# Kernel optimization log

Hardware: AMD Instinct MI355X
Metric: run time of the kernel (lower is better)

Reference implementation:

```python
import jax, jax.numpy as jnp
import numpy as np

B, C, N, L, LAYERS = 32, 128, 307, 12, 4
LH = L + 1  # high-frequency channel time length after left-pad
BN_EPS = 1e-5


def _temporal_attention(seq, c1w, c2w, w, b, v, gamma, beta):
    # seq: [B, C, N, T]
    # conv1 (1x1 over channel dim) -> f1: [B, T, N]
    f1 = jnp.einsum('bcnt,c->btn', seq, c1w)
    # conv2 (1x1 over node dim)    -> f2: [B, T, C]
    f2 = jnp.einsum('bcnt,n->btc', seq, c2w)
    # scores = sigmoid(f1 @ w @ f2^T + b): [B, T, T]
    f1w = jnp.einsum('btn,nc->btc', f1, w)
    scores = jax.nn.sigmoid(jnp.einsum('btc,bqc->btq', f1w, f2) + b)
    # learned mixing: v @ scores
    logits = jnp.einsum('tk,bkq->btq', v, scores)
    # BatchNorm1d over tem_size channels (channel = last axis q after the
    # permute(0,2,1) in the torch code); training-mode batch statistics
    mean = logits.mean(axis=(0, 1), keepdims=True)
    var = ((logits - mean) ** 2).mean(axis=(0, 1), keepdims=True)
    logits = (logits - mean) * jax.lax.rsqrt(var + BN_EPS) * gamma + beta
    coefs = jax.nn.softmax(logits, axis=-1)  # [B, T, Q]
    # x_1 = einsum('bcnl,blq->bcnq', seq, coefs^T)
    return jnp.einsum('bcnt,bqt->bcnq', seq, coefs)


def _make_params(key, c, n, t, layers):
    ks = jax.random.split(key, 4)
    return dict(
        c1=jax.random.normal(ks[0], (layers, c), jnp.float32) * 0.05,
        c2=jax.random.normal(ks[1], (layers, n), jnp.float32) * 0.05,
        w=jax.random.normal(ks[2], (layers, n, c), jnp.float32) * 0.05,
        b=jnp.zeros((layers, t, t), jnp.float32),
        v=jax.random.normal(ks[3], (layers, t, t), jnp.float32) * 0.2,
        g=jnp.ones((layers, t), jnp.float32),
        beta=jnp.zeros((layers, t), jnp.float32),
    )


def setup_inputs():
    key = jax.random.key(0)
    k0, k1, k2, k3 = jax.random.split(key, 4)
    XL = jax.random.normal(k0, (B, C, N, L), jnp.float32)
    XH = jax.random.normal(k1, (B, C, N, L), jnp.float32)
    low = _make_params(k2, C, N, L, LAYERS)
    high = _make_params(k3, C, N, LH, LAYERS)
    return {
        'XL': XL, 'XH': XH,
        'low_c1': low['c1'], 'low_c2': low['c2'], 'low_w': low['w'],
        'low_b': low['b'], 'low_v': low['v'], 'low_g': low['g'], 'low_beta': low['beta'],
        'high_c1': high['c1'], 'high_c2': high['c2'], 'high_w': high['w'],
        'high_b': high['b'], 'high_v': high['v'], 'high_g': high['g'], 'high_beta': high['beta'],
        'alpha': jnp.array(-5.0, jnp.float32),
    }


def reference(XL, XH, low_c1, low_c2, low_w, low_b, low_v, low_g, low_beta,
              high_c1, high_c2, high_w, high_b, high_v, high_g, high_beta, alpha):
    res_xl, res_xh = XL, XH
    x = XL
    for i in range(LAYERS):
        x = _temporal_attention(x, low_c1[i], low_c2[i], low_w[i], low_b[i],
                                low_v[i], low_g[i], low_beta[i])
    xl = (res_xl[..., -1] + x[..., -1])[..., None]  # [B, C, N, 1]

    y = jnp.pad(XH, ((0, 0), (0, 0), (0, 0), (1, 0)))  # left-pad time -> [B,C,N,L+1]
    for i in range(LAYERS):
        y = _temporal_attention(y, high_c1[i], high_c2[i], high_w[i], high_b[i],
                                high_v[i], high_g[i], high_beta[i])
    xh = (res_xh[..., -1] + y[..., -1])[..., None]  # [B, C, N, 1]

    a = jax.nn.sigmoid(alpha)
    return a * xl + (1.0 - a) * xh
```

## Files before the change

### kernel.cpp

```cpp
#include <hip/hip_runtime.h>

#define Bn 32
#define Cc 128
#define Nn 307
#define Ll 12
#define LH 13
#define LAYERS 4
#define BN_EPS 1e-5f
#define SCW (Cc + 1)
#define G1SZ ((size_t)2 * LAYERS * Bn * LH * Nn)
#define NF4 921

__global__ __launch_bounds__(256) void k_g1(const float* __restrict__ XL,
                                            const float* __restrict__ XH,
                                            const float* __restrict__ lc1,
                                            const float* __restrict__ hc1,
                                            float* __restrict__ G1) {
    __shared__ float s_c1t[Cc * 4];
    int bx = blockIdx.x;
    int ft = bx & 3, cs = bx >> 2;
    int b = blockIdx.y, ch = blockIdx.z;
    const float* X = ch ? XH : XL;
    const float* c1 = ch ? hc1 : lc1;
    int tid = threadIdx.x;
    for (int j = tid; j < Cc * 4; j += 256) s_c1t[j] = c1[(j & 3) * Cc + (j >> 2)];
    __syncthreads();
    int f = ft * 256 + tid;
    bool act = f < NF4;
    int cbase = cs * 64;
    float4 a0 = {0.f, 0.f, 0.f, 0.f}, a1 = a0, a2 = a0, a3 = a0;
#define FMA16(xq, cidx)                                                        \
    {                                                                          \
        float4 wq = *(const float4*)&s_c1t[(cbase + (cidx)) * 4];              \
        a0.x += xq.x * wq.x; a0.y += xq.y * wq.x; a0.z += xq.z * wq.x; a0.w += xq.w * wq.x; \
        a1.x += xq.x * wq.y; a1.y += xq.y * wq.y; a1.z += xq.z * wq.y; a1.w += xq.w * wq.y; \
        a2.x += xq.x * wq.z; a2.y += xq.y * wq.z; a2.z += xq.z * wq.z; a2.w += xq.w * wq.z; \
        a3.x += xq.x * wq.w; a3.y += xq.y * wq.w; a3.z += xq.z * wq.w; a3.w += xq.w * wq.w; \
    }
    if (act) {
        const float4* px = (const float4*)X + (size_t)(b * Cc + cbase) * NF4 + f;
        float4 q0 = px[0], q1 = px[NF4], q2 = px[2 * NF4], q3 = px[3 * NF4];
        px += 4 * NF4;
        for (int c = 0; c < 56; c += 4) {
            FMA16(q0, c);     q0 = px[0];
            FMA16(q1, c + 1); q1 = px[NF4];
            FMA16(q2, c + 2); q2 = px[2 * NF4];
            FMA16(q3, c + 3); q3 = px[3 * NF4];
            px += 4 * NF4;
        }
        FMA16(q0, 56); float4 r0 = px[0];
        FMA16(q1, 57); float4 r1 = px[NF4];
        FMA16(q2, 58); float4 r2 = px[2 * NF4];
        FMA16(q3, 59); float4 r3 = px[3 * NF4];
        FMA16(r0, 60); FMA16(r1, 61); FMA16(r2, 62); FMA16(r3, 63);
    }
#undef FMA16
    float* Gout = G1 + (size_t)cs * G1SZ;
    if (act) {
        int tg = f % 3, nn = f / 3;
        int t0b = 4 * tg + ch;
        size_t base = ((size_t)(ch * LAYERS) * Bn + b) * (LH * Nn) + (size_t)t0b * Nn + nn;
        const size_t ls = (size_t)Bn * LH * Nn;
        Gout[base + 0 * ls + 0 * Nn] = a0.x; Gout[base + 0 * ls + 1 * Nn] = a0.y;
        Gout[base + 0 * ls + 2 * Nn] = a0.z; Gout[base + 0 * ls + 3 * Nn] = a0.w;
        Gout[base + 1 * ls + 0 * Nn] = a1.x; Gout[base + 1 * ls + 1 * Nn] = a1.y;
        Gout[base + 1 * ls + 2 * Nn] = a1.z; Gout[base + 1 * ls + 3 * Nn] = a1.w;
        Gout[base + 2 * ls + 0 * Nn] = a2.x; Gout[base + 2 * ls + 1 * Nn] = a2.y;
        Gout[base + 2 * ls + 2 * Nn] = a2.z; Gout[base + 2 * ls + 3 * Nn] = a2.w;
        Gout[base + 3 * ls + 0 * Nn] = a3.x; Gout[base + 3 * ls + 1 * Nn] = a3.y;
        Gout[base + 3 * ls + 2 * Nn] = a3.z; Gout[base + 3 * ls + 3 * Nn] = a3.w;
    }
    int n0 = (ft * 256) / 3;
    int n1 = (ft * 256 + 255) / 3; if (n1 > 306) n1 = 306;
    int cnt = n1 - n0 + 1;
    int t0z = ch ? 0 : (LH - 1);
    for (int o = tid; o < 4 * cnt; o += 256) {
        int l = o / cnt, nn = n0 + o % cnt;
        Gout[((size_t)(ch * LAYERS + l) * Bn + b) * (LH * Nn) + (size_t)t0z * Nn + nn] = 0.f;
    }
}

__global__ __launch_bounds__(192) void k_g2(const float* __restrict__ XL,
                                            const float* __restrict__ XH,
                                            const float* __restrict__ lc2,
                                            const float* __restrict__ hc2,
                                            float* __restrict__ G2) {
    __shared__ float s_c2t[Nn * 4];
    __shared__ float sred2[4 * 12 * 64];
    int c = blockIdx.x, b = blockIdx.y, ch = blockIdx.z;
    const float* X = ch ? XH : XL;
    const float* c2 = ch ? hc2 : lc2;
    int tid = threadIdx.x;
    for (int j = tid; j < Nn * 4; j += 192) s_c2t[j] = c2[(j & 3) * Nn + (j >> 2)];
    __syncthreads();
    const float4* pb = (const float4*)X + (size_t)(b * Cc + c) * NF4;
    float4 x0 = pb[tid];
    float4 x1 = pb[tid + 192];
    float4 x2 = pb[tid + 384];
    float4 x3 = pb[tid + 576];
    float4 x4 = {0.f, 0.f, 0.f, 0.f};
    if (tid + 768 < NF4) x4 = pb[tid + 768];
    float4 a0 = {0.f, 0.f, 0.f, 0.f}, a1 = a0, a2 = a0, a3 = a0;
#define PROC(xq, ff)                                                           \
    {                                                                          \
        int n = (ff) / 3; if (n > 306) n = 306;                                \
        float4 wq = *(const float4*)&s_c2t[n * 4];                             \
        a0.x += xq.x * wq.x; a0.y += xq.y * wq.x; a0.z += xq.z * wq.x; a0.w += xq.w * wq.x; \
        a1.x += xq.x * wq.y; a1.y += xq.y * wq.y; a1.z += xq.z * wq.y; a1.w += xq.w * wq.y; \
        a2.x += xq.x * wq.z; a2.y += xq.y * wq.z; a2.z += xq.z * wq.z; a2.w += xq.w * wq.z; \
        a3.x += xq.x * wq.w; a3.y += xq.y * wq.w; a3.z += xq.z * wq.w; a3.w += xq.w * wq.w; \
    }
    PROC(x0, tid);
    PROC(x1, tid + 192);
    PROC(x2, tid + 384);
    PROC(x3, tid + 576);
    PROC(x4, tid + 768);
#undef PROC
    int tg = tid % 3, m = tid / 3;
    sred2[(0 * 12 + 4 * tg + 0) * 64 + m] = a0.x;
    sred2[(0 * 12 + 4 * tg + 1) * 64 + m] = a0.y;
    sred2[(0 * 12 + 4 * tg + 2) * 64 + m] = a0.z;
    sred2[(0 * 12 + 4 * tg + 3) * 64 + m] = a0.w;
    sred2[(1 * 12 + 4 * tg + 0) * 64 + m] = a1.x;
    sred2[(1 * 12 + 4 * tg + 1) * 64 + m] = a1.y;
    sred2[(1 * 12 + 4 * tg + 2) * 64 + m] = a1.z;
    sred2[(1 * 12 + 4 * tg + 3) * 64 + m] = a1.w;
    sred2[(2 * 12 + 4 * tg + 0) * 64 + m] = a2.x;
    sred2[(2 * 12 + 4 * tg + 1) * 64 + m] = a2.y;
    sred2[(2 * 12 + 4 * tg + 2) * 64 + m] = a2.z;
    sred2[(2 * 12 + 4 * tg + 3) * 64 + m] = a2.w;
    sred2[(3 * 12 + 4 * tg + 0) * 64 + m] = a3.x;
    sred2[(3 * 12 + 4 * tg + 1) * 64 + m] = a3.y;
    sred2[(3 * 12 + 4 * tg + 2) * 64 + m] = a3.z;
    sred2[(3 * 12 + 4 * tg + 3) * 64 + m] = a3.w;
    __syncthreads();
    if (tid < 48) {
        int l = tid / 12, t = tid % 12;
        const float* r = &sred2[(l * 12 + t) * 64];
        float v = 0.f;
#pragma unroll 16
        for (int k = 0; k < 64; ++k) v += r[k];
        int t0 = t + ch;
        G2[((size_t)(ch * LAYERS + l) * Bn + b) * (LH * Cc) + (size_t)t0 * Cc + c] = v;
    } else if (ch && tid < 52) {
        int l = tid - 48;
        G2[((size_t)(ch * LAYERS + l) * Bn + b) * (LH * Cc) + c] = 0.f;
    }
}

#define GWR 4
__global__ __launch_bounds__(256) void k_gw(const float* __restrict__ lw,
                                            const float* __restrict__ hw,
                                            const float* __restrict__ G1,
                                            float* __restrict__ GW) {
    __shared__ float sG1[GWR * Nn];
    __shared__ float sred[8][GWR][Cc];
    int tile = blockIdx.x;
    int chl = blockIdx.y;
    int ch = chl >> 2, l = chl & 3;
    const float* w = (ch ? hw : lw) + (size_t)l * Nn * Cc;
    size_t g1off = (size_t)chl * Bn * (LH * Nn) + (size_t)tile * GWR * Nn;
    const float4* g1a = (const float4*)(G1 + g1off);
    const float4* g1b = (const float4*)(G1 + G1SZ + g1off);
    int tid = threadIdx.x;
    for (int i = tid; i < GWR * Nn / 4; i += 256) {
        float4 pa = g1a[i], pb = g1b[i];
        float4 s = {pa.x + pb.x, pa.y + pb.y, pa.z + pb.z, pa.w + pb.w};
        ((float4*)sG1)[i] = s;
    }
    __syncthreads();
    int c4 = (tid & 31) * 4;
    int stripe = tid >> 5;
    float4 a0 = {0.f, 0.f, 0.f, 0.f}, a1 = a0, a2 = a0, a3 = a0;
#define GW_FMA(wv, nn)                                         \
    {                                                          \
        float g0 = sG1[0 * Nn + (nn)];                         \
        float g1v = sG1[1 * Nn + (nn)];                        \
        float g2v = sG1[2 * Nn + (nn)];                        \
        float g3v = sG1[3 * Nn + (nn)];                        \
        a0.x += wv.x * g0;  a0.y += wv.y * g0;                 \
        a0.z += wv.z * g0;  a0.w += wv.w * g0;                 \
        a1.x += wv.x * g1v; a1.y += wv.y * g1v;                \
        a1.z += wv.z * g1v; a1.w += wv.w * g1v;                \
        a2.x += wv.x * g2v; a2.y += wv.y * g2v;                \
        a2.z += wv.z * g2v; a2.w += wv.w * g2v;                \
        a3.x += wv.x * g3v; a3.y += wv.y * g3v;                \
        a3.z += wv.z * g3v; a3.w += wv.w * g3v;                \
    }
    int n = stripe;
    for (; n + 24 < Nn; n += 32) {
        float4 w0 = *(const float4*)(w + (size_t)n * Cc + c4);
        float4 w1 = *(const float4*)(w + (size_t)(n + 8) * Cc + c4);
        float4 w2 = *(const float4*)(w + (size_t)(n + 16) * Cc + c4);
        float4 w3 = *(const float4*)(w + (size_t)(n + 24) * Cc + c4);
        GW_FMA(w0, n);
        GW_FMA(w1, n + 8);
        GW_FMA(w2, n + 16);
        GW_FMA(w3, n + 24);
    }
    for (; n < Nn; n += 8) {
        float4 w0 = *(const float4*)(w + (size_t)n * Cc + c4);
        GW_FMA(w0, n);
    }
#undef GW_FMA
    *(float4*)&sred[stripe][0][c4] = a0;
    *(float4*)&sred[stripe][1][c4] = a1;
    *(float4*)&sred[stripe][2][c4] = a2;
    *(float4*)&sred[stripe][3][c4] = a3;
    __syncthreads();
    float* out = GW + (size_t)chl * Bn * (LH * Cc) + (size_t)tile * GWR * Cc;
    for (int o = tid; o < GWR * Cc; o += 256) {
        int r = o >> 7, cc = o & 127;
        float v = 0.f;
#pragma unroll
        for (int s = 0; s < 8; ++s) v += sred[s][r][cc];
        out[o] = v;
    }
}

__global__ __launch_bounds__(256) void k_m(const float* __restrict__ GW,
                                           const float* __restrict__ G2,
                                           float* __restrict__ M) {
    __shared__ float sGW[LH][SCW];
    __shared__ float sG2[LH][SCW];
    int blk = blockIdx.x;
    int ch = blk >> 7;
    int T = ch ? LH : Ll;
    const float* gw = GW + (size_t)blk * (LH * Cc);
    const float* g2 = G2 + (size_t)blk * (LH * Cc);
    int tid = threadIdx.x;
    for (int i = tid; i < LH * Cc; i += 256) {
        int t = i >> 7, c = i & 127;
        sGW[t][c] = gw[i];
        sG2[t][c] = g2[i];
    }
    __syncthreads();
    float* Mo = M + (size_t)blk * (LH * LH);
    for (int i = tid; i < T * T; i += 256) {
        int t0 = i / T, t1 = i % T;
        float a = 0.f;
#pragma unroll 8
        for (int cc = 0; cc < Cc; ++cc) a += sGW[t0][cc] * sG2[t1][cc];
        Mo[t0 * LH + t1] = a;
    }
}

template <int T>
__device__ __forceinline__ void first_impl(int ch, int b,
                                           const float* __restrict__ M,
                                           const float* __restrict__ bb,
                                           const float* __restrict__ v,
                                           float* __restrict__ Lg,
                                           float* __restrict__ Stats) {
    const int TT = T * T;
    __shared__ float sS[LH * LH];
    __shared__ float sA[LH * LH];
    int tid = threadIdx.x;
    const float* Ml = M + ((size_t)(ch * LAYERS + 0) * Bn + b) * (LH * LH);
    if (tid < TT) {
        int t = tid / T, q = tid % T;
        float a = bb[tid] + Ml[t * LH + q];
        sS[tid] = 1.f / (1.f + expf(-a));
    }
    __syncthreads();
    if (tid < TT) {
        int t = tid / T, q = tid % T;
        float a = 0.f;
#pragma unroll
        for (int k = 0; k < T; ++k) a += v[t * T + k] * sS[k * T + q];
        sA[tid] = a;
        Lg[(size_t)(ch * Bn + b) * (LH * LH) + tid] = a;
    }
    __syncthreads();
    if (tid < T) {
        float s = 0.f, ss = 0.f;
#pragma unroll
        for (int t = 0; t < T; ++t) {
            float x = sA[t * T + tid];
            s += x;
            ss += x * x;
        }
        float* St = Stats + (size_t)(0 * 2 + ch) * 2 * (LH * Bn);
        St[tid * Bn + b] = s;
        St[LH * Bn + tid * Bn + b] = ss;
    }
}

__global__ __launch_bounds__(192) void k_first(const float* __restrict__ M,
                                               const float* __restrict__ lb,
                                               const float* __restrict__ lv,
                                               const float* __restrict__ hb,
                                               const float* __restrict__ hv,
                                               float* __restrict__ Lg,
                                               float* __restrict__ Stats) {
    int ch = blockIdx.x >> 5, b = blockIdx.x & 31;
    if (ch == 0)
        first_impl<Ll>(0, b, M, lb, lv, Lg, Stats);
    else
        first_impl<LH>(1, b, M, hb, hv, Lg, Stats);
}

template <int T>
__device__ __forceinline__ void mid_impl(int ch, int b, int l,
                                         const float* __restrict__ M,
                                         const float* __restrict__ bb_all,
                                         const float* __restrict__ v_all,
                                         const float* __restrict__ g_all,
                                         const float* __restrict__ be_all,
                                         float* __restrict__ Lg,
                                         float* __restrict__ Stats,
                                         float* __restrict__ Pws) {
    const int TT = T * T;
    __shared__ float sP[LH * LH], sC[LH * LH], sA[LH * LH], sB[LH * LH], sM[LH * LH];
    __shared__ float sMean[LH], sScale[LH], sShift[LH];
    int tid = threadIdx.x;
    bool first = (l == 0);
    float* Lgb = Lg + (size_t)(ch * Bn + b) * (LH * LH);
    float* Pb = Pws + (size_t)(ch * Bn + b) * (LH * LH);
    if (tid < T) {
        const float* St = Stats + (size_t)(l * 2 + ch) * 2 * (LH * Bn);
        float s = 0.f, ss = 0.f;
        for (int b2 = 0; b2 < Bn; ++b2) {
            s += St[tid * Bn + b2];
            ss += St[LH * Bn + tid * Bn + b2];
        }
        float inv = 1.f / (float)(Bn * T);
        float m = s * inv;
        float var = ss * inv - m * m;
        sMean[tid] = m;
        sScale[tid] = rsqrtf(var + BN_EPS) * g_all[l * T + tid];
        sShift[tid] = be_all[l * T + tid];
    }
    if (tid < TT) {
        sA[tid] = Lgb[tid];
        if (!first) sP[tid] = Pb[tid];
    }
    __syncthreads();
    if (tid < T) {
        float vals[T];
        float mx = -1e30f;
#pragma unroll
        for (int q = 0; q < T; ++q) {
            float x = (sA[tid * T + q] - sMean[q]) * sScale[q] + sShift[q];
            vals[q] = x;
            mx = fmaxf(mx, x);
        }
        float sm = 0.f;
#pragma unroll
        for (int q = 0; q < T; ++q) {
            vals[q] = expf(vals[q] - mx);
            sm += vals[q];
        }
        float inv = 1.f / sm;
#pragma unroll
        for (int q = 0; q < T; ++q) sC[tid * T + q] = vals[q] * inv;
    }
    __syncthreads();
    if (tid < TT) {
        int t0 = tid / T, q = tid % T;
        float a;
        if (first) {
            a = sC[q * T + t0];
        } else {
            a = 0.f;
#pragma unroll
            for (int t = 0; t < T; ++t) a += sP[t0 * T + t] * sC[q * T + t];
        }
        sB[tid] = a;
        Pb[tid] = a;
    }
    const float* Mn = M + ((size_t)(ch * LAYERS + l + 1) * Bn + b) * (LH * LH);
    for (int i = tid; i < T * LH; i += 192) sM[i] = Mn[i];
    __syncthreads();
    if (tid < TT) {
        int t = tid / T, t1 = tid % T;
        float a = 0.f;
#pragma unroll
        for (int t0 = 0; t0 < T; ++t0) a += sB[t0 * T + t] * sM[t0 * LH + t1];
        sA[tid] = a;
    }
    __syncthreads();
    const float* bbn = bb_all + (size_t)(l + 1) * TT;
    if (tid < TT) {
        int t = tid / T, q = tid % T;
        float a = bbn[tid];
#pragma unroll
        for (int t1 = 0; t1 < T; ++t1) a += sA[t * T + t1] * sB[t1 * T + q];
        sP[tid] = 1.f / (1.f + expf(-a));
    }
    __syncthreads();
    const float* vn = v_all + (size_t)(l + 1) * TT;
    if (tid < TT) {
        int t = tid / T, q = tid % T;
        float a = 0.f;
#pragma unroll
        for (int k = 0; k < T; ++k) a += vn[t * T + k] * sP[k * T + q];
        sA[tid] = a;
        Lgb[tid] = a;
    }
    __syncthreads();
    if (tid < T) {
        float s = 0.f, ss = 0.f;
#pragma unroll
        for (int t = 0; t < T; ++t) {
            float x = sA[t * T + tid];
            s += x;
            ss += x * x;
        }
        float* St = Stats + (size_t)((l + 1) * 2 + ch) * 2 * (LH * Bn);
        St[tid * Bn + b] = s;
        St[LH * Bn + tid * Bn + b] = ss;
    }
}

__global__ __launch_bounds__(192) void k_mid(const float* __restrict__ M,
                                             const float* __restrict__ lb,
                                             const float* __restrict__ lv,
                                             const float* __restrict__ lgam,
                                             const float* __restrict__ lbet,
                                             const float* __restrict__ hb,
                                             const float* __restrict__ hv,
                                             const float* __restrict__ hgam,
                                             const float* __restrict__ hbet,
                                             float* __restrict__ Lg,
                                             float* __restrict__ Stats,
                                             float* __restrict__ Pws, int l) {
    int ch = blockIdx.x >> 5, b = blockIdx.x & 31;
    if (ch == 0)
        mid_impl<Ll>(0, b, l, M, lb, lv, lgam, lbet, Lg, Stats, Pws);
    else
        mid_impl<LH>(1, b, l, M, hb, hv, hgam, hbet, Lg, Stats, Pws);
}

template <int T>
__device__ __forceinline__ void last_impl(int ch, int b,
                                          const float* __restrict__ g_all,
                                          const float* __restrict__ be_all,
                                          const float* __restrict__ Lg,
                                          const float* __restrict__ Stats,
                                          const float* __restrict__ Pws,
                                          float* __restrict__ Pcol) {
    const int TT = T * T;
    const int l = LAYERS - 1;
    __shared__ float sP[LH * LH], sC[LH * LH], sA[LH * LH], sB[LH * LH];
    __shared__ float sMean[LH], sScale[LH], sShift[LH];
    int tid = threadIdx.x;
    const float* Lgb = Lg + (size_t)(ch * Bn + b) * (LH * LH);
    const float* Pb = Pws + (size_t)(ch * Bn + b) * (LH * LH);
    if (tid < T) {
        const float* St = Stats + (size_t)(l * 2 + ch) * 2 * (LH * Bn);
        float s = 0.f, ss = 0.f;
        for (int b2 = 0; b2 < Bn; ++b2) {
            s += St[tid * Bn + b2];
            ss += St[LH * Bn + tid * Bn + b2];
        }
        float inv = 1.f / (float)(Bn * T);
        float m = s * inv;
        float var = ss * inv - m * m;
        sMean[tid] = m;
        sScale[tid] = rsqrtf(var + BN_EPS) * g_all[l * T + tid];
        sShift[tid] = be_all[l * T + tid];
    }
    if (tid < TT) {
        sA[tid] = Lgb[tid];
        sP[tid] = Pb[tid];
    }
    __syncthreads();
    if (tid < T) {
        float vals[T];
        float mx = -1e30f;
#pragma unroll
        for (int q = 0; q < T; ++q) {
            float x = (sA[tid * T + q] - sMean[q]) * sScale[q] + sShift[q];
            vals[q] = x;
            mx = fmaxf(mx, x);
        }
        float sm = 0.f;
#pragma unroll
        for (int q = 0; q < T; ++q) {
            vals[q] = expf(vals[q] - mx);
            sm += vals[q];
        }
        float inv = 1.f / sm;
#pragma unroll
        for (int q = 0; q < T; ++q) sC[tid * T + q] = vals[q] * inv;
    }
    __syncthreads();
    if (tid < TT) {
        int t0 = tid / T, q = tid % T;
        float a = 0.f;
#pragma unroll
        for (int t = 0; t < T; ++t) a += sP[t0 * T + t] * sC[q * T + t];
        sB[tid] = a;
    }
    __syncthreads();
    if (tid < T) Pcol[(size_t)ch * Bn * LH + b * LH + tid] = sB[tid * T + (T - 1)];
}

__global__ __launch_bounds__(192) void k_last(const float* __restrict__ lgam,
                                              const float* __restrict__ lbet,
                                              const float* __restrict__ hgam,
                                              const float* __restrict__ hbet,
                                              const float* __restrict__ Lg,
                                              const float* __restrict__ Stats,
                                              const float* __restrict__ Pws,
                                              float* __restrict__ Pcol) {
    int ch = blockIdx.x >> 5, b = blockIdx.x & 31;
    if (ch == 0)
        last_impl<Ll>(0, b, lgam, lbet, Lg, Stats, Pws, Pcol);
    else
        last_impl<LH>(1, b, hgam, hbet, Lg, Stats, Pws, Pcol);
}

__global__ __launch_bounds__(192) void k_final(const float* __restrict__ XL,
                                               const float* __restrict__ XH,
                                               const float* __restrict__ Pcol,
                                               const float* __restrict__ alpha,
                                               float* __restrict__ out) {
    __shared__ float s_pl[Ll];
    __shared__ float s_ph[LH];
    __shared__ float sfin[192];
    int b = blockIdx.y;
    int tid = threadIdx.x;
    if (tid < Ll) s_pl[tid] = Pcol[b * LH + tid];
    if (tid >= 64 && tid < 64 + LH) s_ph[tid - 64] = Pcol[Bn * LH + b * LH + (tid - 64)];
    __syncthreads();
    int F = blockIdx.x * 192 + tid;
    int tg = F % 3;
    const float4* pl4 = (const float4*)XL + (size_t)b * (Cc * Nn * 3) + F;
    const float4* ph4 = (const float4*)XH + (size_t)b * (Cc * Nn * 3) + F;
    float4 xl = *pl4;
    float4 xh = *ph4;
    float a = 1.f / (1.f + expf(-alpha[0]));
    const float* wl = &s_pl[4 * tg];
    const float* wh = &s_ph[4 * tg + 1];
    float pL = xl.x * wl[0] + xl.y * wl[1] + xl.z * wl[2] + xl.w * wl[3];
    float pH = xh.x * wh[0] + xh.y * wh[1] + xh.z * wh[2] + xh.w * wh[3];
    float p = a * pL + (1.f - a) * pH;
    if (tg == 2) p += a * xl.w + (1.f - a) * xh.w;
    sfin[tid] = p;
    __syncthreads();
    if (tid < 64) {
        float v = sfin[3 * tid] + sfin[3 * tid + 1] + sfin[3 * tid + 2];
        out[(size_t)b * (Cc * Nn) + blockIdx.x * 64 + tid] = v;
    }
}

extern "C" void kernel_launch(void* const* d_in, const int* in_sizes, int n_in,
                              void* d_out, int out_size, void* d_ws, size_t ws_size,
                              hipStream_t stream) {
    const float* XL = (const float*)d_in[0];
    const float* XH = (const float*)d_in[1];
    const float* lc1 = (const float*)d_in[2];
    const float* lc2 = (const float*)d_in[3];
    const float* lw = (const float*)d_in[4];
    const float* lb = (const float*)d_in[5];
    const float* lv = (const float*)d_in[6];
    const float* lg = (const float*)d_in[7];
    const float* lbeta = (const float*)d_in[8];
    const float* hc1 = (const float*)d_in[9];
    const float* hc2 = (const float*)d_in[10];
    const float* hw = (const float*)d_in[11];
    const float* hb = (const float*)d_in[12];
    const float* hv = (const float*)d_in[13];
    const float* hg = (const float*)d_in[14];
    const float* hbeta = (const float*)d_in[15];
    const float* alpha = (const float*)d_in[16];
    float* out = (float*)d_out;

    float* ws = (float*)d_ws;
    float* G1 = ws;
    float* G2 = G1 + 2 * G1SZ;
    float* M = G2 + (size_t)2 * LAYERS * Bn * LH * Cc;
    float* Pcol = M + (size_t)2 * LAYERS * Bn * LH * LH;
    float* Stats = Pcol + (size_t)2 * Bn * LH;
    float* Lg = Stats + (size_t)4 * LAYERS * LH * Bn;
    float* Pws = Lg + (size_t)2 * Bn * LH * LH;
    float* GW = Pws + (size_t)2 * Bn * LH * LH;

    k_g1<<<dim3(8, 32, 2), 256, 0, stream>>>(XL, XH, lc1, hc1, G1);
    k_g2<<<dim3(128, 32, 2), 192, 0, stream>>>(XL, XH, lc2, hc2, G2);
    k_gw<<<dim3(104, 8), 256, 0, stream>>>(lw, hw, G1, GW);
    k_m<<<256, 256, 0, stream>>>(GW, G2, M);
    k_first<<<64, 192, 0, stream>>>(M, lb, lv, hb, hv, Lg, Stats);
    k_mid<<<64, 192, 0, stream>>>(M, lb, lv, lg, lbeta, hb, hv, hg, hbeta, Lg, Stats, Pws, 0);
    k_mid<<<64, 192, 0, stream>>>(M, lb, lv, lg, lbeta, hb, hv, hg, hbeta, Lg, Stats, Pws, 1);
    k_mid<<<64, 192, 0, stream>>>(M, lb, lv, lg, lbeta, hb, hv, hg, hbeta, Lg, Stats, Pws, 2);
    k_last<<<64, 192, 0, stream>>>(lg, lbeta, hg, hbeta, Lg, Stats, Pws, Pcol);
    k_final<<<dim3(614, 32), 192, 0, stream>>>(XL, XH, Pcol, alpha, out);
}
```

Measured before the change: 256.5 us.

## Merge G1/G2 projection kernels and fold first-layer score step into k_m

Combines the two input-projection kernels into one launch: blocks with bx<10 compute the channel reduction (G1), now using 192 threads per block and 8-deep load prefetching, while the other blocks compute the node reduction (G2). The first-layer sigmoid/mixing/statistics step is folded into k_m for the layer-0 blocks, so the k_first launch is removed. This cuts two kernel launches and lets the two memory-bound passes over X run concurrently. In exchange, G1 now runs as 10 blocks per (b,ch) instead of 8, and k_m's layer-0 blocks do extra serial work.

```diff
diff --git a/kernel.cpp b/kernel.cpp
--- a/kernel.cpp
+++ b/kernel.cpp
@@ -11,24 +11,28 @@
 #define G1SZ ((size_t)2 * LAYERS * Bn * LH * Nn)
 #define NF4 921
 
-__global__ __launch_bounds__(256) void k_g1(const float* __restrict__ XL,
+__global__ __launch_bounds__(192) void k_gx(const float* __restrict__ XL,
                                             const float* __restrict__ XH,
                                             const float* __restrict__ lc1,
                                             const float* __restrict__ hc1,
-                                            float* __restrict__ G1) {
-    __shared__ float s_c1t[Cc * 4];
+                                            const float* __restrict__ lc2,
+                                            const float* __restrict__ hc2,
+                                            float* __restrict__ G1,
+                                            float* __restrict__ G2) {
     int bx = blockIdx.x;
-    int ft = bx & 3, cs = bx >> 2;
     int b = blockIdx.y, ch = blockIdx.z;
     const float* X = ch ? XH : XL;
-    const float* c1 = ch ? hc1 : lc1;
     int tid = threadIdx.x;
-    for (int j = tid; j < Cc * 4; j += 256) s_c1t[j] = c1[(j & 3) * Cc + (j >> 2)];
-    __syncthreads();
-    int f = ft * 256 + tid;
-    bool act = f < NF4;
-    int cbase = cs * 64;
-    float4 a0 = {0.f, 0.f, 0.f, 0.f}, a1 = a0, a2 = a0, a3 = a0;
+    if (bx < 10) {
+        __shared__ float s_c1t[Cc * 4];
+        const float* c1 = ch ? hc1 : lc1;
+        int ft = bx % 5, cs = bx / 5;
+        for (int j = tid; j < Cc * 4; j += 192) s_c1t[j] = c1[(j & 3) * Cc + (j >> 2)];
+        __syncthreads();
+        int f = ft * 192 + tid;
+        bool act = f < NF4;
+        int cbase = cs * 64;
+        float4 a0 = {0.f, 0.f, 0.f, 0.f}, a1 = a0, a2 = a0, a3 = a0;
 #define FMA16(xq, cidx)                                                        \
     {                                                                          \
         float4 wq = *(const float4*)&s_c1t[(cbase + (cidx)) * 4];              \
@@ -37,70 +41,72 @@
         a2.x += xq.x * wq.z; a2.y += xq.y * wq.z; a2.z += xq.z * wq.z; a2.w += xq.w * wq.z; \
         a3.x += xq.x * wq.w; a3.y += xq.y * wq.w; a3.z += xq.z * wq.w; a3.w += xq.w * wq.w; \
     }
-    if (act) {
-        const float4* px = (const float4*)X + (size_t)(b * Cc + cbase) * NF4 + f;
-        float4 q0 = px[0], q1 = px[NF4], q2 = px[2 * NF4], q3 = px[3 * NF4];
-        px += 4 * NF4;
-        for (int c = 0; c < 56; c += 4) {
-            FMA16(q0, c);     q0 = px[0];
-            FMA16(q1, c + 1); q1 = px[NF4];
-            FMA16(q2, c + 2); q2 = px[2 * NF4];
-            FMA16(q3, c + 3); q3 = px[3 * NF4];
-            px += 4 * NF4;
-        }
-        FMA16(q0, 56); float4 r0 = px[0];
-        FMA16(q1, 57); float4 r1 = px[NF4];
-        FMA16(q2, 58); float4 r2 = px[2 * NF4];
-        FMA16(q3, 59); float4 r3 = px[3 * NF4];
-        FMA16(r0, 60); FMA16(r1, 61); FMA16(r2, 62); FMA16(r3, 63);
-    }
+        if (act) {
+            const float4* px = (const float4*)X + (size_t)(b * Cc + cbase) * NF4 + f;
+            float4 q0 = px[0 * NF4], q1 = px[1 * NF4], q2 = px[2 * NF4], q3 = px[3 * NF4];
+            float4 q4 = px[4 * NF4], q5 = px[5 * NF4], q6 = px[6 * NF4], q7 = px[7 * NF4];
+            px += 8 * NF4;
+            for (int c = 0; c < 48; c += 8) {
+                FMA16(q0, c + 0); q0 = px[0 * NF4];
+                FMA16(q1, c + 1); q1 = px[1 * NF4];
+                FMA16(q2, c + 2); q2 = px[2 * NF4];
+                FMA16(q3, c + 3); q3 = px[3 * NF4];
+                FMA16(q4, c + 4); q4 = px[4 * NF4];
+                FMA16(q5, c + 5); q5 = px[5 * NF4];
+                FMA16(q6, c + 6); q6 = px[6 * NF4];
+                FMA16(q7, c + 7); q7 = px[7 * NF4];
+                px += 8 * NF4;
+            }
+            FMA16(q0, 48); q0 = px[0 * NF4];
+            FMA16(q1, 49); q1 = px[1 * NF4];
+            FMA16(q2, 50); q2 = px[2 * NF4];
+            FMA16(q3, 51); q3 = px[3 * NF4];
+            FMA16(q4, 52); q4 = px[4 * NF4];
+            FMA16(q5, 53); q5 = px[5 * NF4];
+            FMA16(q6, 54); q6 = px[6 * NF4];
+            FMA16(q7, 55); q7 = px[7 * NF4];
+            FMA16(q0, 56); FMA16(q1, 57); FMA16(q2, 58); FMA16(q3, 59);
+            FMA16(q4, 60); FMA16(q5, 61); FMA16(q6, 62); FMA16(q7, 63);
+        }
 #undef FMA16
-    float* Gout = G1 + (size_t)cs * G1SZ;
-    if (act) {
-        int tg = f % 3, nn = f / 3;
-        int t0b = 4 * tg + ch;
-        size_t base = ((size_t)(ch * LAYERS) * Bn + b) * (LH * Nn) + (size_t)t0b * Nn + nn;
-        const size_t ls = (size_t)Bn * LH * Nn;
-        Gout[base + 0 * ls + 0 * Nn] = a0.x; Gout[base + 0 * ls + 1 * Nn] = a0.y;
-        Gout[base + 0 * ls + 2 * Nn] = a0.z; Gout[base + 0 * ls + 3 * Nn] = a0.w;
-        Gout[base + 1 * ls + 0 * Nn] = a1.x; Gout[base + 1 * ls + 1 * Nn] = a1.y;
-        Gout[base + 1 * ls + 2 * Nn] = a1.z; Gout[base + 1 * ls + 3 * Nn] = a1.w;
-        Gout[base + 2 * ls + 0 * Nn] = a2.x; Gout[base + 2 * ls + 1 * Nn] = a2.y;
-        Gout[base + 2 * ls + 2 * Nn] = a2.z; Gout[base + 2 * ls + 3 * Nn] = a2.w;
-        Gout[base + 3 * ls + 0 * Nn] = a3.x; Gout[base + 3 * ls + 1 * Nn] = a3.y;
-        Gout[base + 3 * ls + 2 * Nn] = a3.z; Gout[base + 3 * ls + 3 * Nn] = a3.w;
-    }
-    int n0 = (ft * 256) / 3;
-    int n1 = (ft * 256 + 255) / 3; if (n1 > 306) n1 = 306;
-    int cnt = n1 - n0 + 1;
-    int t0z = ch ? 0 : (LH - 1);
-    for (int o = tid; o < 4 * cnt; o += 256) {
-        int l = o / cnt, nn = n0 + o % cnt;
-        Gout[((size_t)(ch * LAYERS + l) * Bn + b) * (LH * Nn) + (size_t)t0z * Nn + nn] = 0.f;
-    }
-}
-
-__global__ __launch_bounds__(192) void k_g2(const float* __restrict__ XL,
-                                            const float* __restrict__ XH,
-                                            const float* __restrict__ lc2,
-                                            const float* __restrict__ hc2,
-                                            float* __restrict__ G2) {
-    __shared__ float s_c2t[Nn * 4];
-    __shared__ float sred2[4 * 12 * 64];
-    int c = blockIdx.x, b = blockIdx.y, ch = blockIdx.z;
-    const float* X = ch ? XH : XL;
-    const float* c2 = ch ? hc2 : lc2;
-    int tid = threadIdx.x;
-    for (int j = tid; j < Nn * 4; j += 192) s_c2t[j] = c2[(j & 3) * Nn + (j >> 2)];
-    __syncthreads();
-    const float4* pb = (const float4*)X + (size_t)(b * Cc + c) * NF4;
-    float4 x0 = pb[tid];
-    float4 x1 = pb[tid + 192];
-    float4 x2 = pb[tid + 384];
-    float4 x3 = pb[tid + 576];
-    float4 x4 = {0.f, 0.f, 0.f, 0.f};
-    if (tid + 768 < NF4) x4 = pb[tid + 768];
-    float4 a0 = {0.f, 0.f, 0.f, 0.f}, a1 = a0, a2 = a0, a3 = a0;
+        float* Gout = G1 + (size_t)cs * G1SZ;
+        if (act) {
+            int tg = f % 3, nn = f / 3;
+            int t0b = 4 * tg + ch;
+            size_t base = ((size_t)(ch * LAYERS) * Bn + b) * (LH * Nn) + (size_t)t0b * Nn + nn;
+            const size_t ls = (size_t)Bn * LH * Nn;
+            Gout[base + 0 * ls + 0 * Nn] = a0.x; Gout[base + 0 * ls + 1 * Nn] = a0.y;
+            Gout[base + 0 * ls + 2 * Nn] = a0.z; Gout[base + 0 * ls + 3 * Nn] = a0.w;
+            Gout[base + 1 * ls + 0 * Nn] = a1.x; Gout[base + 1 * ls + 1 * Nn] = a1.y;
+            Gout[base + 1 * ls + 2 * Nn] = a1.z; Gout[base + 1 * ls + 3 * Nn] = a1.w;
+            Gout[base + 2 * ls + 0 * Nn] = a2.x; Gout[base + 2 * ls + 1 * Nn] = a2.y;
+            Gout[base + 2 * ls + 2 * Nn] = a2.z; Gout[base + 2 * ls + 3 * Nn] = a2.w;
+            Gout[base + 3 * ls + 0 * Nn] = a3.x; Gout[base + 3 * ls + 1 * Nn] = a3.y;
+            Gout[base + 3 * ls + 2 * Nn] = a3.z; Gout[base + 3 * ls + 3 * Nn] = a3.w;
+        }
+        int n0 = ft * 64;
+        int n1 = ft * 64 + 63; if (n1 > 306) n1 = 306;
+        int cnt = n1 - n0 + 1;
+        int t0z = ch ? 0 : (LH - 1);
+        for (int o = tid; o < 4 * cnt; o += 192) {
+            int l = o / cnt, nn = n0 + o % cnt;
+            Gout[((size_t)(ch * LAYERS + l) * Bn + b) * (LH * Nn) + (size_t)t0z * Nn + nn] = 0.f;
+        }
+    } else {
+        __shared__ float s_c2t[Nn * 4];
+        __shared__ float sred2[4 * 12 * 64];
+        int c = bx - 10;
+        const float* c2 = ch ? hc2 : lc2;
+        for (int j = tid; j < Nn * 4; j += 192) s_c2t[j] = c2[(j & 3) * Nn + (j >> 2)];
+        __syncthreads();
+        const float4* pb = (const float4*)X + (size_t)(b * Cc + c) * NF4;
+        float4 x0 = pb[tid];
+        float4 x1 = pb[tid + 192];
+        float4 x2 = pb[tid + 384];
+        float4 x3 = pb[tid + 576];
+        float4 x4 = {0.f, 0.f, 0.f, 0.f};
+        if (tid + 768 < NF4) x4 = pb[tid + 768];
+        float4 a0 = {0.f, 0.f, 0.f, 0.f}, a1 = a0, a2 = a0, a3 = a0;
 #define PROC(xq, ff)                                                           \
     {                                                                          \
         int n = (ff) / 3; if (n > 306) n = 306;                                \
@@ -110,41 +116,42 @@
         a2.x += xq.x * wq.z; a2.y += xq.y * wq.z; a2.z += xq.z * wq.z; a2.w += xq.w * wq.z; \
         a3.x += xq.x * wq.w; a3.y += xq.y * wq.w; a3.z += xq.z * wq.w; a3.w += xq.w * wq.w; \
     }
-    PROC(x0, tid);
-    PROC(x1, tid + 192);
-    PROC(x2, tid + 384);
-    PROC(x3, tid + 576);
-    PROC(x4, tid + 768);
+        PROC(x0, tid);
+        PROC(x1, tid + 192);
+        PROC(x2, tid + 384);
+        PROC(x3, tid + 576);
+        PROC(x4, tid + 768);
 #undef PROC
-    int tg = tid % 3, m = tid / 3;
-    sred2[(0 * 12 + 4 * tg + 0) * 64 + m] = a0.x;
-    sred2[(0 * 12 + 4 * tg + 1) * 64 + m] = a0.y;
-    sred2[(0 * 12 + 4 * tg + 2) * 64 + m] = a0.z;
-    sred2[(0 * 12 + 4 * tg + 3) * 64 + m] = a0.w;
-    sred2[(1 * 12 + 4 * tg + 0) * 64 + m] = a1.x;
-    sred2[(1 * 12 + 4 * tg + 1) * 64 + m] = a1.y;
-    sred2[(1 * 12 + 4 * tg + 2) * 64 + m] = a1.z;
-    sred2[(1 * 12 + 4 * tg + 3) * 64 + m] = a1.w;
-    sred2[(2 * 12 + 4 * tg + 0) * 64 + m] = a2.x;
-    sred2[(2 * 12 + 4 * tg + 1) * 64 + m] = a2.y;
-    sred2[(2 * 12 + 4 * tg + 2) * 64 + m] = a2.z;
-    sred2[(2 * 12 + 4 * tg + 3) * 64 + m] = a2.w;
-    sred2[(3 * 12 + 4 * tg + 0) * 64 + m] = a3.x;
-    sred2[(3 * 12 + 4 * tg + 1) * 64 + m] = a3.y;
-    sred2[(3 * 12 + 4 * tg + 2) * 64 + m] = a3.z;
-    sred2[(3 * 12 + 4 * tg + 3) * 64 + m] = a3.w;
-    __syncthreads();
-    if (tid < 48) {
-        int l = tid / 12, t = tid % 12;
-        const float* r = &sred2[(l * 12 + t) * 64];
-        float v = 0.f;
+        int tg = tid % 3, m = tid / 3;
+        sred2[(0 * 12 + 4 * tg + 0) * 64 + m] = a0.x;
+        sred2[(0 * 12 + 4 * tg + 1) * 64 + m] = a0.y;
+        sred2[(0 * 12 + 4 * tg + 2) * 64 + m] = a0.z;
+        sred2[(0 * 12 + 4 * tg + 3) * 64 + m] = a0.w;
+        sred2[(1 * 12 + 4 * tg + 0) * 64 + m] = a1.x;
+        sred2[(1 * 12 + 4 * tg + 1) * 64 + m] = a1.y;
+        sred2[(1 * 12 + 4 * tg + 2) * 64 + m] = a1.z;
+        sred2[(1 * 12 + 4 * tg + 3) * 64 + m] = a1.w;
+        sred2[(2 * 12 + 4 * tg + 0) * 64 + m] = a2.x;
+        sred2[(2 * 12 + 4 * tg + 1) * 64 + m] = a2.y;
+        sred2[(2 * 12 + 4 * tg + 2) * 64 + m] = a2.z;
+        sred2[(2 * 12 + 4 * tg + 3) * 64 + m] = a2.w;
+        sred2[(3 * 12 + 4 * tg + 0) * 64 + m] = a3.x;
+        sred2[(3 * 12 + 4 * tg + 1) * 64 + m] = a3.y;
+        sred2[(3 * 12 + 4 * tg + 2) * 64 + m] = a3.z;
+        sred2[(3 * 12 + 4 * tg + 3) * 64 + m] = a3.w;
+        __syncthreads();
+        if (tid < 48) {
+            int l = tid / 12, t = tid % 12;
+            const float* r = &sred2[(l * 12 + t) * 64];
+            float v = 0.f;
 #pragma unroll 16
-        for (int k = 0; k < 64; ++k) v += r[k];
-        int t0 = t + ch;
-        G2[((size_t)(ch * LAYERS + l) * Bn + b) * (LH * Cc) + (size_t)t0 * Cc + c] = v;
-    } else if (ch && tid < 52) {
-        int l = tid - 48;
-        G2[((size_t)(ch * LAYERS + l) * Bn + b) * (LH * Cc) + c] = 0.f;
+            for (int k = 0; k < 64; ++k) v += r[k];
+            int t0 = t + ch;
+            G2[((size_t)(ch * LAYERS + l) * Bn + b) * (LH * Cc) + (size_t)t0 * Cc + c] = v;
+        } else if (ch && tid < 52) {
+            int l = tid - 48;
+            G2[((size_t)(ch * LAYERS + l) * Bn + b) * (LH * Cc) + c] = 0.f;
+        }
     }
 }
 
@@ -220,11 +227,22 @@
 
 __global__ __launch_bounds__(256) void k_m(const float* __restrict__ GW,
                                            const float* __restrict__ G2,
-                                           float* __restrict__ M) {
+                                           const float* __restrict__ lb,
+                                           const float* __restrict__ lv,
+                                           const float* __restrict__ hb,
+                                           const float* __restrict__ hv,
+                                           float* __restrict__ M,
+                                           float* __restrict__ Lg,
+                                           float* __restrict__ Stats) {
     __shared__ float sGW[LH][SCW];
     __shared__ float sG2[LH][SCW];
+    __shared__ float sMm[LH * LH];
+    __shared__ float sS[LH * LH];
+    __shared__ float sA[LH * LH];
     int blk = blockIdx.x;
     int ch = blk >> 7;
+    int l = (blk >> 5) & 3;
+    int b = blk & 31;
     int T = ch ? LH : Ll;
     const float* gw = GW + (size_t)blk * (LH * Cc);
     const float* g2 = G2 + (size_t)blk * (LH * Cc);
@@ -236,37 +254,28 @@
     }
     __syncthreads();
     float* Mo = M + (size_t)blk * (LH * LH);
-    for (int i = tid; i < T * T; i += 256) {
-        int t0 = i / T, t1 = i % T;
+    if (tid < T * T) {
+        int t0 = tid / T, t1 = tid % T;
         float a = 0.f;
 #pragma unroll 8
         for (int cc = 0; cc < Cc; ++cc) a += sGW[t0][cc] * sG2[t1][cc];
         Mo[t0 * LH + t1] = a;
-    }
-}
-
-template <int T>
-__device__ __forceinline__ void first_impl(int ch, int b,
-                                           const float* __restrict__ M,
-                                           const float* __restrict__ bb,
-                                           const float* __restrict__ v,
-                                           float* __restrict__ Lg,
-                                           float* __restrict__ Stats) {
-    const int TT = T * T;
-    __shared__ float sS[LH * LH];
-    __shared__ float sA[LH * LH];
-    int tid = threadIdx.x;
-    const float* Ml = M + ((size_t)(ch * LAYERS + 0) * Bn + b) * (LH * LH);
+        sMm[t0 * LH + t1] = a;
+    }
+    if (l != 0) return;
+    const float* bb = ch ? hb : lb;
+    const float* v = ch ? hv : lv;
+    __syncthreads();
+    int TT = T * T;
     if (tid < TT) {
         int t = tid / T, q = tid % T;
-        float a = bb[tid] + Ml[t * LH + q];
+        float a = bb[tid] + sMm[t * LH + q];
         sS[tid] = 1.f / (1.f + expf(-a));
     }
     __syncthreads();
     if (tid < TT) {
         int t = tid / T, q = tid % T;
         float a = 0.f;
-#pragma unroll
         for (int k = 0; k < T; ++k) a += v[t * T + k] * sS[k * T + q];
         sA[tid] = a;
         Lg[(size_t)(ch * Bn + b) * (LH * LH) + tid] = a;
@@ -274,7 +283,6 @@
     __syncthreads();
     if (tid < T) {
         float s = 0.f, ss = 0.f;
-#pragma unroll
         for (int t = 0; t < T; ++t) {
             float x = sA[t * T + tid];
             s += x;
@@ -284,20 +292,6 @@
         St[tid * Bn + b] = s;
         St[LH * Bn + tid * Bn + b] = ss;
     }
-}
-
-__global__ __launch_bounds__(192) void k_first(const float* __restrict__ M,
-                                               const float* __restrict__ lb,
-                                               const float* __restrict__ lv,
-                                               const float* __restrict__ hb,
-                                               const float* __restrict__ hv,
-                                               float* __restrict__ Lg,
-                                               float* __restrict__ Stats) {
-    int ch = blockIdx.x >> 5, b = blockIdx.x & 31;
-    if (ch == 0)
-        first_impl<Ll>(0, b, M, lb, lv, Lg, Stats);
-    else
-        first_impl<LH>(1, b, M, hb, hv, Lg, Stats);
 }
 
 template <int T>
@@ -578,11 +572,9 @@
     float* Pws = Lg + (size_t)2 * Bn * LH * LH;
     float* GW = Pws + (size_t)2 * Bn * LH * LH;
 
-    k_g1<<<dim3(8, 32, 2), 256, 0, stream>>>(XL, XH, lc1, hc1, G1);
-    k_g2<<<dim3(128, 32, 2), 192, 0, stream>>>(XL, XH, lc2, hc2, G2);
+    k_gx<<<dim3(138, 32, 2), 192, 0, stream>>>(XL, XH, lc1, hc1, lc2, hc2, G1, G2);
     k_gw<<<dim3(104, 8), 256, 0, stream>>>(lw, hw, G1, GW);
-    k_m<<<256, 256, 0, stream>>>(GW, G2, M);
-    k_first<<<64, 192, 0, stream>>>(M, lb, lv, hb, hv, Lg, Stats);
+    k_m<<<256, 256, 0, stream>>>(GW, G2, lb, lv, hb, hv, M, Lg, Stats);
     k_mid<<<64, 192, 0, stream>>>(M, lb, lv, lg, lbeta, hb, hv, hg, hbeta, Lg, Stats, Pws, 0);
     k_mid<<<64, 192, 0, stream>>>(M, lb, lv, lg, lbeta, hb, hv, hg, hbeta, Lg, Stats, Pws, 1);
     k_mid<<<64, 192, 0, stream>>>(M, lb, lv, lg, lbeta, hb, hv, hg, hbeta, Lg, Stats, Pws, 2);
```

New measurement: 233.3 us. 9.0% less time.
